# Kernel tuning notes

Hardware: AMD Instinct MI355X
Metric: run time of the kernel (lower is better)

Reference implementation:

```python
import jax, jax.numpy as jnp
import numpy as np

N, D, OUT = 8192, 512, 1


def setup_inputs() -> dict:
    key = jax.random.key(0)
    ks = jax.random.split(key, 6)
    # Glorot-normal-ish scales (stddev = sqrt(2/(fan_in+fan_out)))
    s_mat = np.sqrt(2.0 / (D + OUT)).astype(np.float32)
    s_vec = np.sqrt(2.0 / (OUT + 1)).astype(np.float32)
    return {
        "x": jax.random.normal(ks[0], (N, D), dtype=jnp.float32),
        "mu_kernel": jax.random.normal(ks[1], (D, OUT), dtype=jnp.float32) * s_mat,
        "rho_kernel": jax.random.normal(ks[2], (OUT,), dtype=jnp.float32) * s_vec,
        "var_kernel": jax.random.normal(ks[3], (D, OUT), dtype=jnp.float32) * s_mat,
        "mu_bias": jax.random.normal(ks[4], (OUT,), dtype=jnp.float32) * s_vec,
        "var_bias": jax.random.normal(ks[5], (OUT,), dtype=jnp.float32) * s_vec,
    }


def reference(x, mu_kernel, rho_kernel, var_kernel, mu_bias, var_bias):
    # mean head: [N, 1]
    output_mu = x @ mu_kernel + mu_bias
    # diagonal variances: softplus(x @ W + b) + eps, squeezed to [N]
    d = jnp.log1p(jnp.exp(x @ var_kernel + var_bias))[:, 0] + 1e-8
    # rho[i,j] = sum_k x[i,k] * x[j,k] * rho_kernel  (rho_kernel is scalar-broadcast)
    # == (x * rho_kernel) @ x^T  -- avoids the O(N^2*D) tiled intermediate
    rho = (x * rho_kernel[0]) @ x.T  # [N, N]
    n = x.shape[0]
    idx = jnp.arange(n)
    output_cov = rho.at[idx, idx].set(d)
    return output_mu, output_cov
```

## Files before the change

### kernel.cpp

```cpp
#include <hip/hip_runtime.h>
#include <hip/hip_bf16.h>

#define NROWS 8192
#define DDIM  512

typedef __bf16 bf16x8 __attribute__((ext_vector_type(8)));
typedef float  f32x4  __attribute__((ext_vector_type(4)));

__device__ __forceinline__ void gload_lds16(const void* g, void* l) {
    __builtin_amdgcn_global_load_lds((const __attribute__((address_space(1))) void*)g,
                                     (__attribute__((address_space(3))) void*)l,
                                     16, 0, 0);
}

__global__ __launch_bounds__(256) void prep_kernel(
    const float* __restrict__ x,
    const float* __restrict__ mu_k,
    const float* __restrict__ var_k,
    const float* __restrict__ mu_b,
    const float* __restrict__ var_b,
    float* __restrict__ mu_out,
    float* __restrict__ d_vec,
    __hip_bfloat16* __restrict__ xb)
{
    const int lane = threadIdx.x & 63;
    const int row  = blockIdx.x * 4 + (threadIdx.x >> 6);
    const int k0   = lane * 8;

    const float4* xr = reinterpret_cast<const float4*>(x + (size_t)row * DDIM + k0);
    float4 a = xr[0];
    float4 b = xr[1];
    const float* mk = mu_k + k0;
    const float* vk = var_k + k0;

    float dm = a.x*mk[0] + a.y*mk[1] + a.z*mk[2] + a.w*mk[3]
             + b.x*mk[4] + b.y*mk[5] + b.z*mk[6] + b.w*mk[7];
    float dv = a.x*vk[0] + a.y*vk[1] + a.z*vk[2] + a.w*vk[3]
             + b.x*vk[4] + b.y*vk[5] + b.z*vk[6] + b.w*vk[7];

    union { __hip_bfloat16 h[8]; uint4 u; } pk;
    pk.h[0] = __float2bfloat16(a.x);
    pk.h[1] = __float2bfloat16(a.y);
    pk.h[2] = __float2bfloat16(a.z);
    pk.h[3] = __float2bfloat16(a.w);
    pk.h[4] = __float2bfloat16(b.x);
    pk.h[5] = __float2bfloat16(b.y);
    pk.h[6] = __float2bfloat16(b.z);
    pk.h[7] = __float2bfloat16(b.w);
    *reinterpret_cast<uint4*>(xb + (size_t)row * DDIM + k0) = pk.u;

    #pragma unroll
    for (int off = 32; off; off >>= 1) {
        dm += __shfl_xor(dm, off);
        dv += __shfl_xor(dv, off);
    }
    if (lane == 0) {
        mu_out[row] = dm + mu_b[0];
        float z = dv + var_b[0];
        d_vec[row] = fmaxf(z, 0.0f) + log1pf(expf(-fabsf(z))) + 1e-8f;
    }
}

__global__ __launch_bounds__(256) void syrk_kernel(
    const __hip_bfloat16* __restrict__ xb,
    const float* __restrict__ d_vec,
    const float* __restrict__ rho_k,
    float* __restrict__ cov)
{
    __shared__ __align__(16) char smem[64 * 133 * 4];
    __hip_bfloat16* As = reinterpret_cast<__hip_bfloat16*>(smem);
    __hip_bfloat16* Bs = reinterpret_cast<__hip_bfloat16*>(smem + 16384);
    float* T = reinterpret_cast<float*>(smem);

    const int bid = blockIdx.x;
    int bi = (int)(64.5f - sqrtf(64.5f * 64.5f - 2.0f * (float)bid));
    if (bi < 0) bi = 0;
    if (bi > 63) bi = 63;
    while ((bi + 1) * 64 - ((bi + 1) * bi) / 2 <= bid) ++bi;
    while (bi * 64 - (bi * (bi - 1)) / 2 > bid) --bi;
    const int bj = bi + (bid - (bi * 64 - (bi * (bi - 1)) / 2));

    const int tid  = threadIdx.x;
    const int lane = tid & 63;
    const int w    = tid >> 6;
    const int wr   = w >> 1, wc = w & 1;
    const size_t arow0 = (size_t)bi * 128;
    const size_t brow0 = (size_t)bj * 128;

    f32x4 acc[4][4] = {};

    const int srow = lane >> 3;
    const int scol = (lane & 7) * 8;

    for (int kt = 0; kt < DDIM; kt += 64) {
        #pragma unroll
        for (int i = 0; i < 4; ++i) {
            const int loff = i * 4096 + w * 1024;
            const int row  = i * 32 + w * 8 + srow;
            gload_lds16(xb + (arow0 + row) * DDIM + kt + scol, (char*)As + loff);
            gload_lds16(xb + (brow0 + row) * DDIM + kt + scol, (char*)Bs + loff);
        }
        __syncthreads();

        #pragma unroll
        for (int ks = 0; ks < 2; ++ks) {
            bf16x8 af[4], bfr[4];
            const int cb = ks * 64 + (lane >> 4) * 16;
            #pragma unroll
            for (int m = 0; m < 4; ++m) {
                const int r = wr * 64 + m * 16 + (lane & 15);
                af[m] = *reinterpret_cast<const bf16x8*>((const char*)As + r * 128 + cb);
            }
            #pragma unroll
            for (int n = 0; n < 4; ++n) {
                const int r = wc * 64 + n * 16 + (lane & 15);
                bfr[n] = *reinterpret_cast<const bf16x8*>((const char*)Bs + r * 128 + cb);
            }
            #pragma unroll
            for (int m = 0; m < 4; ++m)
                #pragma unroll
                for (int n = 0; n < 4; ++n)
                    acc[m][n] = __builtin_amdgcn_mfma_f32_16x16x32_bf16(
                        af[m], bfr[n], acc[m][n], 0, 0, 0);
        }
        __syncthreads();
    }

    const float s = rho_k[0];
    const bool isDiag = (bi == bj);
    const size_t gr0 = arow0 + wr * 64 + (lane >> 4) * 4;
    const size_t gc0 = brow0 + wc * 64 + (lane & 15);

    if (isDiag) {
        #pragma unroll
        for (int m = 0; m < 4; ++m)
            #pragma unroll
            for (int n = 0; n < 4; ++n) {
                const size_t col = gc0 + n * 16;
                #pragma unroll
                for (int r = 0; r < 4; ++r) {
                    const size_t row = gr0 + m * 16 + r;
                    float v = acc[m][n][r] * s;
                    if (row == col) v = d_vec[row];
                    cov[row * (size_t)NROWS + col] = v;
                }
            }
    } else {
        #pragma unroll
        for (int m = 0; m < 4; ++m)
            #pragma unroll
            for (int n = 0; n < 4; ++n) {
                const size_t col = gc0 + n * 16;
                #pragma unroll
                for (int r = 0; r < 4; ++r) {
                    const size_t row = gr0 + m * 16 + r;
                    cov[row * (size_t)NROWS + col] = acc[m][n][r] * s;
                }
            }

        #pragma unroll
        for (int h = 0; h < 2; ++h) {
            __syncthreads();
            if (wr == h) {
                #pragma unroll
                for (int m = 0; m < 4; ++m)
                    #pragma unroll
                    for (int n = 0; n < 4; ++n) {
                        const int c = wc * 64 + n * 16 + (lane & 15);
                        #pragma unroll
                        for (int r = 0; r < 4; ++r) {
                            const int rp = m * 16 + (lane >> 4) * 4 + r;
                            T[rp * 133 + c] = acc[m][n][r] * s;
                        }
                    }
            }
            __syncthreads();
            #pragma unroll
            for (int it = 0; it < 8; ++it) {
                const int chunk = it * 256 + tid;
                const int c  = chunk >> 4;
                const int r0 = (chunk & 15) * 4;
                float4 v;
                v.x = T[(r0 + 0) * 133 + c];
                v.y = T[(r0 + 1) * 133 + c];
                v.z = T[(r0 + 2) * 133 + c];
                v.w = T[(r0 + 3) * 133 + c];
                *reinterpret_cast<float4*>(
                    &cov[(brow0 + c) * (size_t)NROWS + arow0 + h * 64 + r0]) = v;
            }
        }
    }
}

extern "C" void kernel_launch(void* const* d_in, const int* in_sizes, int n_in,
                              void* d_out, int out_size, void* d_ws, size_t ws_size,
                              hipStream_t stream) {
    const float* x     = (const float*)d_in[0];
    const float* mu_k  = (const float*)d_in[1];
    const float* rho_k = (const float*)d_in[2];
    const float* var_k = (const float*)d_in[3];
    const float* mu_b  = (const float*)d_in[4];
    const float* var_b = (const float*)d_in[5];

    float* out    = (float*)d_out;
    float* mu_out = out;
    float* cov    = out + NROWS;

    __hip_bfloat16* xb = (__hip_bfloat16*)d_ws;
    float* d_vec = (float*)((char*)d_ws + (size_t)NROWS * DDIM * 2);

    prep_kernel<<<NROWS / 4, 256, 0, stream>>>(x, mu_k, var_k, mu_b, var_b,
                                               mu_out, d_vec, xb);

    syrk_kernel<<<2080, 256, 0, stream>>>(xb, d_vec, rho_k, cov);
}
```

Before: 335.0 us.

## Load MFMA fragments directly from global with register double buffering and swizzle block order

Drops the LDS staging of A/B tiles and loads bf16 fragments straight from global memory into registers, double-buffered across k-steps, which removes the barriers from the main loop. It also remaps block IDs so that consecutive workgroups spread across 8 chunks of the triangular tile list, probably to balance XCD/L2 locality. The trade-off is more register pressure and uncoalesced 16-byte global loads that rely on the cache for reuse. The kernel is mostly bound by writing the 256MB output, so the compute-side change may matter little.

```diff
diff --git a/kernel.cpp b/kernel.cpp
--- a/kernel.cpp
+++ b/kernel.cpp
@@ -6,12 +6,6 @@
 
 typedef __bf16 bf16x8 __attribute__((ext_vector_type(8)));
 typedef float  f32x4  __attribute__((ext_vector_type(4)));
-
-__device__ __forceinline__ void gload_lds16(const void* g, void* l) {
-    __builtin_amdgcn_global_load_lds((const __attribute__((address_space(1))) void*)g,
-                                     (__attribute__((address_space(3))) void*)l,
-                                     16, 0, 0);
-}
 
 __global__ __launch_bounds__(256) void prep_kernel(
     const float* __restrict__ x,
@@ -67,12 +61,10 @@
     const float* __restrict__ rho_k,
     float* __restrict__ cov)
 {
-    __shared__ __align__(16) char smem[64 * 133 * 4];
-    __hip_bfloat16* As = reinterpret_cast<__hip_bfloat16*>(smem);
-    __hip_bfloat16* Bs = reinterpret_cast<__hip_bfloat16*>(smem + 16384);
-    float* T = reinterpret_cast<float*>(smem);
-
-    const int bid = blockIdx.x;
+    __shared__ __align__(16) float T[64 * 133];
+
+    const int bid = (blockIdx.x % 8) * 260 + (blockIdx.x / 8);
+
     int bi = (int)(64.5f - sqrtf(64.5f * 64.5f - 2.0f * (float)bid));
     if (bi < 0) bi = 0;
     if (bi > 63) bi = 63;
@@ -87,44 +79,51 @@
     const size_t arow0 = (size_t)bi * 128;
     const size_t brow0 = (size_t)bj * 128;
 
+    const int fr = lane & 15;
+    const int kb = (lane >> 4) * 8;
+
+    const __hip_bfloat16* Ab = xb + (arow0 + wr * 64 + fr) * DDIM + kb;
+    const __hip_bfloat16* Bb = xb + (brow0 + wc * 64 + fr) * DDIM + kb;
+
     f32x4 acc[4][4] = {};
 
-    const int srow = lane >> 3;
-    const int scol = (lane & 7) * 8;
-
-    for (int kt = 0; kt < DDIM; kt += 64) {
-        #pragma unroll
-        for (int i = 0; i < 4; ++i) {
-            const int loff = i * 4096 + w * 1024;
-            const int row  = i * 32 + w * 8 + srow;
-            gload_lds16(xb + (arow0 + row) * DDIM + kt + scol, (char*)As + loff);
-            gload_lds16(xb + (brow0 + row) * DDIM + kt + scol, (char*)Bs + loff);
-        }
-        __syncthreads();
-
-        #pragma unroll
-        for (int ks = 0; ks < 2; ++ks) {
-            bf16x8 af[4], bfr[4];
-            const int cb = ks * 64 + (lane >> 4) * 16;
-            #pragma unroll
-            for (int m = 0; m < 4; ++m) {
-                const int r = wr * 64 + m * 16 + (lane & 15);
-                af[m] = *reinterpret_cast<const bf16x8*>((const char*)As + r * 128 + cb);
-            }
-            #pragma unroll
-            for (int n = 0; n < 4; ++n) {
-                const int r = wc * 64 + n * 16 + (lane & 15);
-                bfr[n] = *reinterpret_cast<const bf16x8*>((const char*)Bs + r * 128 + cb);
-            }
-            #pragma unroll
-            for (int m = 0; m < 4; ++m)
-                #pragma unroll
-                for (int n = 0; n < 4; ++n)
-                    acc[m][n] = __builtin_amdgcn_mfma_f32_16x16x32_bf16(
-                        af[m], bfr[n], acc[m][n], 0, 0, 0);
-        }
-        __syncthreads();
-    }
+#define LOADF(AF, BF, KT)                                                        \
+    {                                                                            \
+        _Pragma("unroll")                                                        \
+        for (int ks = 0; ks < 2; ++ks) {                                         \
+            const int ko = (KT) + ks * 32;                                       \
+            _Pragma("unroll")                                                    \
+            for (int m = 0; m < 4; ++m)                                          \
+                AF[ks][m] = *reinterpret_cast<const bf16x8*>(Ab + (size_t)m * 16 * DDIM + ko); \
+            _Pragma("unroll")                                                    \
+            for (int n = 0; n < 4; ++n)                                          \
+                BF[ks][n] = *reinterpret_cast<const bf16x8*>(Bb + (size_t)n * 16 * DDIM + ko); \
+        }                                                                        \
+    }
+
+#define MFMAS(AF, BF)                                                            \
+    {                                                                            \
+        _Pragma("unroll")                                                        \
+        for (int ks = 0; ks < 2; ++ks)                                           \
+            _Pragma("unroll")                                                    \
+            for (int m = 0; m < 4; ++m)                                          \
+                _Pragma("unroll")                                                \
+                for (int n = 0; n < 4; ++n)                                      \
+                    acc[m][n] = __builtin_amdgcn_mfma_f32_16x16x32_bf16(         \
+                        AF[ks][m], BF[ks][n], acc[m][n], 0, 0, 0);               \
+    }
+
+    bf16x8 a0[2][4], b0[2][4], a1[2][4], b1[2][4];
+    LOADF(a0, b0, 0);
+    #pragma unroll
+    for (int kt = 0; kt < DDIM; kt += 128) {
+        LOADF(a1, b1, kt + 64);
+        MFMAS(a0, b0);
+        if (kt + 128 < DDIM) LOADF(a0, b0, kt + 128);
+        MFMAS(a1, b1);
+    }
+#undef LOADF
+#undef MFMAS
 
     const float s = rho_k[0];
     const bool isDiag = (bi == bj);
```

Result: slower. 412.5 us (+23.1%).
